# Kernel optimization log

Measured on AMD Instinct MI355X. Metric: run time of the kernel, lower is better.

Reference implementation:

```python
import jax, jax.numpy as jnp
import numpy as np
import math

B, S, D, H = 2, 2048, 1024, 16

def setup_inputs() -> dict:
    key = jax.random.key(0)
    ks = jax.random.split(key, 13)
    def lin(kw, kb, out_d, in_d):
        W = jax.random.normal(kw, (out_d, in_d), dtype=jnp.float32) * 0.02
        b = jax.random.normal(kb, (out_d,), dtype=jnp.float32) * 0.02
        return W, b
    Wq, bq = lin(ks[0], ks[1], D, D)
    Wk, bk = lin(ks[2], ks[3], D, D)
    Wv, bv = lin(ks[4], ks[5], D, D)
    Wo, bo = lin(ks[6], ks[7], D, D)
    query = jax.random.normal(ks[8], (B, S, D), dtype=jnp.float32)
    key_t = jax.random.normal(ks[9], (B, S, D), dtype=jnp.float32)
    value = jax.random.normal(ks[10], (B, S, D), dtype=jnp.float32)
    src_mask = jax.random.randint(ks[11], (B, S), 0, 2).astype(bool)  # True = masked out
    return {"query": query, "key": key_t, "value": value, "src_mask": src_mask,
            "Wq": Wq, "bq": bq, "Wk": Wk, "bk": bk, "Wv": Wv, "bv": bv,
            "Wo": Wo, "bo": bo, "nhead": H}

def reference(query, key, value, src_mask, Wq, bq, Wk, bk, Wv, bv, Wo, bo, nhead):
    b, s, d = query.shape
    hd = d // nhead
    scale = 1.0 / math.sqrt(hd)
    def split_heads(x):  # [b,s,d] -> [b,h,s,hd]
        return x.reshape(b, -1, nhead, hd).transpose(0, 2, 1, 3)
    q = split_heads(query @ Wq.T + bq)
    k = split_heads(key @ Wk.T + bk)
    v = split_heads(value @ Wv.T + bv)
    scores = jnp.einsum('bhqe,bhke->bhqk', q, k) * scale  # [b,h,s,s]
    # mask True -> -9e9, broadcast over heads and query positions (matches repeat)
    scores = jnp.where(src_mask[:, None, None, :], jnp.float32(-9e9), scores)
    probs = jax.nn.softmax(scores, axis=-1)
    # dropout is identity in eval mode
    out = jnp.einsum('bhqk,bhke->bhqe', probs, v)  # [b,h,s,hd]
    out = out.transpose(0, 2, 1, 3).reshape(b, s, d)
    out = out @ Wo.T + bo
    return out
```

## Files before the change

### kernel.cpp

```cpp
#include <hip/hip_runtime.h>
#include <hip/hip_bf16.h>
#include <cstdint>
#include <cstddef>

#define B_ 2
#define S_ 2048
#define D_ 1024
#define H_ 16
#define HD_ 64
#define M_ 4096

typedef __attribute__((ext_vector_type(8))) short short8;
typedef __attribute__((ext_vector_type(4))) short shortx4;
typedef __attribute__((ext_vector_type(4))) float floatx4;

__device__ __forceinline__ floatx4 mfma32(short8 a, short8 b, floatx4 c) {
    return __builtin_amdgcn_mfma_f32_16x16x32_bf16(a, b, c, 0, 0, 0);
}
__device__ __forceinline__ floatx4 mfma16(shortx4 a, shortx4 b, floatx4 c) {
    return __builtin_amdgcn_mfma_f32_16x16x16bf16_1k(a, b, c, 0, 0, 0);
}

__device__ __forceinline__ void gload_lds16(const __hip_bfloat16* g, __hip_bfloat16* lds_base) {
    __builtin_amdgcn_global_load_lds(
        (const __attribute__((address_space(1))) void*)g,
        (__attribute__((address_space(3))) void*)lds_base, 16, 0, 0);
}

__global__ __launch_bounds__(256) void cvt_all_kernel(
    const float* __restrict__ q, const float* __restrict__ k, const float* __restrict__ v,
    const float* __restrict__ wq, const float* __restrict__ wk,
    const float* __restrict__ wv, const float* __restrict__ wo,
    __hip_bfloat16* __restrict__ dst_in,
    __hip_bfloat16* __restrict__ dst_w)
{
    const size_t SZ_IN = (size_t)M_ * D_;
    const size_t SZ_W  = (size_t)D_ * D_;
    int i = (blockIdx.x * 256 + threadIdx.x) * 4;
    const float* src;
    __hip_bfloat16* d;
    if (blockIdx.z < 3) {
        src = blockIdx.z == 0 ? q : blockIdx.z == 1 ? k : v;
        d = dst_in + (size_t)blockIdx.z * SZ_IN + i;
        src += i;
    } else {
        int w = i >> 20;
        int off = i & (int)(SZ_W - 1);
        src = (w == 0 ? wq : w == 1 ? wk : w == 2 ? wv : wo) + off;
        d = dst_w + (size_t)w * SZ_W + off;
    }
    float4 vv = *(const float4*)src;
    union { __hip_bfloat16 h[4]; uint2 u; } cv;
    cv.h[0] = __float2bfloat16(vv.x); cv.h[1] = __float2bfloat16(vv.y);
    cv.h[2] = __float2bfloat16(vv.z); cv.h[3] = __float2bfloat16(vv.w);
    *(uint2*)d = cv.u;
}

template <int MODE>
__device__ __forceinline__ void gemm_core(
    const __hip_bfloat16* __restrict__ A,
    const __hip_bfloat16* __restrict__ W,
    const float* __restrict__ bias,
    void* __restrict__ Cout,
    __hip_bfloat16* __restrict__ smem,
    int m0, int n0, int N, float scale)
{
    __hip_bfloat16* As = smem;
    __hip_bfloat16* Bs = smem + 128 * 32;
    const int K = D_;
    const int tid  = threadIdx.x;
    const int wave = tid >> 6;
    const int lane = tid & 63;
    const int quad = lane >> 4;
    const int l15  = lane & 15;
    const int wm   = (wave & 1) * 64;
    const int wn   = (wave >> 1) * 64;
    const int srow = lane >> 2;
    const int scol = (lane & 3) * 8;

    floatx4 acc[4][4];
#pragma unroll
    for (int i = 0; i < 4; i++)
#pragma unroll
        for (int j = 0; j < 4; j++) {
            floatx4 z = {0.f, 0.f, 0.f, 0.f};
            acc[i][j] = z;
        }

    for (int k0 = 0; k0 < K; k0 += 32) {
        __syncthreads();
#pragma unroll
        for (int t = 0; t < 2; t++) {
            int r0 = wave * 32 + t * 16;
            gload_lds16(A + (size_t)(m0 + r0 + srow) * K + k0 + scol, As + r0 * 32);
            gload_lds16(W + (size_t)(n0 + r0 + srow) * K + k0 + scol, Bs + r0 * 32);
        }
        __syncthreads();

        short8 afr[4], bfr[4];
#pragma unroll
        for (int i = 0; i < 4; i++)
            afr[i] = *(const short8*)(As + (wm + i * 16 + l15) * 32 + quad * 8);
#pragma unroll
        for (int j = 0; j < 4; j++)
            bfr[j] = *(const short8*)(Bs + (wn + j * 16 + l15) * 32 + quad * 8);
#pragma unroll
        for (int i = 0; i < 4; i++)
#pragma unroll
            for (int j = 0; j < 4; j++)
                acc[i][j] = mfma32(afr[i], bfr[j], acc[i][j]);
    }

    if constexpr (MODE == 1) {
#pragma unroll
        for (int j = 0; j < 4; j++) {
            int col = n0 + wn + j * 16 + l15;
            int h = col >> 6, e = col & 63;
            float bv = bias[col];
#pragma unroll
            for (int i = 0; i < 4; i++) {
                int s0 = m0 + wm + i * 16 + quad * 4;
                int bb = s0 >> 11, sl = s0 & 2047;
                union { __hip_bfloat16 hx[4]; uint2 u; } pk;
#pragma unroll
                for (int r = 0; r < 4; r++)
                    pk.hx[r] = __float2bfloat16(acc[i][j][r] + bv);
                *(uint2*)((__hip_bfloat16*)Cout + (((size_t)bb * H_ + h) * HD_ + e) * S_ + sl) = pk.u;
            }
        }
    } else {
#pragma unroll
        for (int j = 0; j < 4; j++) {
            int col = n0 + wn + j * 16 + l15;
            float bv = bias[col];
#pragma unroll
            for (int i = 0; i < 4; i++) {
#pragma unroll
                for (int r = 0; r < 4; r++) {
                    int rowg = m0 + wm + i * 16 + quad * 4 + r;
                    ((__hip_bfloat16*)Cout)[(size_t)rowg * N + col] =
                        __float2bfloat16((acc[i][j][r] + bv) * scale);
                }
            }
        }
    }
}

__global__ __launch_bounds__(256) void qkv_gemm_kernel(
    const __hip_bfloat16* __restrict__ qb, const __hip_bfloat16* __restrict__ kb,
    const __hip_bfloat16* __restrict__ vb,
    const __hip_bfloat16* __restrict__ Wqb, const __hip_bfloat16* __restrict__ Wkb,
    const __hip_bfloat16* __restrict__ Wvb,
    const float* __restrict__ bq, const float* __restrict__ bk, const float* __restrict__ bv,
    __hip_bfloat16* __restrict__ Qp, __hip_bfloat16* __restrict__ Kp,
    __hip_bfloat16* __restrict__ Vt)
{
    __shared__ __hip_bfloat16 smem[2 * 128 * 32] __attribute__((aligned(16)));
    const int z = blockIdx.z;
    const __hip_bfloat16* A = z == 0 ? qb : z == 1 ? kb : vb;
    const __hip_bfloat16* W = z == 0 ? Wqb : z == 1 ? Wkb : Wvb;
    const float* bias = z == 0 ? bq : z == 1 ? bk : bv;
    int m0 = blockIdx.y * 128, n0 = blockIdx.x * 128;
    const float kSc = 0.18033688f;
    if (z < 2) gemm_core<0>(A, W, bias, z == 0 ? (void*)Qp : (void*)Kp, smem, m0, n0, D_,
                            z == 0 ? kSc : 1.0f);
    else       gemm_core<1>(A, W, bias, (void*)Vt, smem, m0, n0, D_, 1.0f);
}

__global__ __launch_bounds__(256) void oproj_gemm_kernel(
    const __hip_bfloat16* __restrict__ A, const __hip_bfloat16* __restrict__ W,
    const float* __restrict__ bias, float* __restrict__ out)
{
    __shared__ __hip_bfloat16 As[64 * 32]  __attribute__((aligned(16)));
    __shared__ __hip_bfloat16 Bs[128 * 32] __attribute__((aligned(16)));
    const int K = D_, N = D_;
    const int tid  = threadIdx.x;
    const int m0   = blockIdx.y * 64;
    const int n0   = blockIdx.x * 128;
    const int wave = tid >> 6;
    const int lane = tid & 63;
    const int quad = lane >> 4;
    const int l15  = lane & 15;
    const int wm   = (wave & 1) * 32;
    const int wn   = (wave >> 1) * 64;
    const int srow = lane >> 2;
    const int scol = (lane & 3) * 8;

    floatx4 acc[2][4];
#pragma unroll
    for (int i = 0; i < 2; i++)
#pragma unroll
        for (int j = 0; j < 4; j++) {
            floatx4 z = {0.f, 0.f, 0.f, 0.f};
            acc[i][j] = z;
        }

    for (int k0 = 0; k0 < K; k0 += 32) {
        __syncthreads();
        {
            int ra = wave * 16;
            gload_lds16(A + (size_t)(m0 + ra + srow) * K + k0 + scol, As + ra * 32);
#pragma unroll
            for (int t = 0; t < 2; t++) {
                int rb = wave * 32 + t * 16;
                gload_lds16(W + (size_t)(n0 + rb + srow) * K + k0 + scol, Bs + rb * 32);
            }
        }
        __syncthreads();

        short8 afr[2], bfr[4];
#pragma unroll
        for (int i = 0; i < 2; i++)
            afr[i] = *(const short8*)(As + (wm + i * 16 + l15) * 32 + quad * 8);
#pragma unroll
        for (int j = 0; j < 4; j++)
            bfr[j] = *(const short8*)(Bs + (wn + j * 16 + l15) * 32 + quad * 8);
#pragma unroll
        for (int i = 0; i < 2; i++)
#pragma unroll
            for (int j = 0; j < 4; j++)
                acc[i][j] = mfma32(afr[i], bfr[j], acc[i][j]);
    }

#pragma unroll
    for (int j = 0; j < 4; j++) {
        int col = n0 + wn + j * 16 + l15;
        float bv = bias[col];
#pragma unroll
        for (int i = 0; i < 2; i++) {
#pragma unroll
            for (int r = 0; r < 4; r++) {
                int rowg = m0 + wm + i * 16 + quad * 4 + r;
                out[(size_t)rowg * N + col] = acc[i][j][r] + bv;
            }
        }
    }
}

#define LDP 72
__global__ __launch_bounds__(512) void flash_attn_kernel(
    const __hip_bfloat16* __restrict__ Q,
    const __hip_bfloat16* __restrict__ Kp,
    const __hip_bfloat16* __restrict__ Vt,
    const int* __restrict__ mask,
    __hip_bfloat16* __restrict__ O)
{
    __shared__ __hip_bfloat16 Qs [128 * LDP] __attribute__((aligned(16)));
    __shared__ __hip_bfloat16 Ks [64 * LDP]  __attribute__((aligned(16)));
    __shared__ __hip_bfloat16 Vts[64 * LDP]  __attribute__((aligned(16)));

    const int tid  = threadIdx.x;
    const int q0   = blockIdx.x * 128;
    const int bh   = blockIdx.y;
    const int b    = bh >> 4;
    const int h    = bh & 15;
    const int wave = tid >> 6;
    const int lane = tid & 63;
    const int quad = lane >> 4;
    const int l15  = lane & 15;

    const size_t baseQ = ((size_t)b * S_ + q0) * D_ + (size_t)h * HD_;
#pragma unroll
    for (int c = tid; c < 1024; c += 512) {
        int row = c >> 3, kc = c & 7;
        *(uint4*)(Qs + row * LDP + kc * 8) = *(const uint4*)(Q + baseQ + (size_t)row * D_ + kc * 8);
    }
    __syncthreads();

    short8 qb[2];
    qb[0] = *(const short8*)(Qs + (wave * 16 + l15) * LDP + quad * 8);
    qb[1] = *(const short8*)(Qs + (wave * 16 + l15) * LDP + 32 + quad * 8);

    const shortx4 ones = {(short)0x3F80, (short)0x3F80, (short)0x3F80, (short)0x3F80};
    floatx4 l_acc = {0.f, 0.f, 0.f, 0.f};
    floatx4 o_acc[4];
#pragma unroll
    for (int ot = 0; ot < 4; ot++) {
        floatx4 z = {0.f, 0.f, 0.f, 0.f};
        o_acc[ot] = z;
    }

    const int* mrow = mask + b * S_;
    const __hip_bfloat16* VtBase = Vt + (size_t)bh * HD_ * S_;

    for (int kv0 = 0; kv0 < S_; kv0 += 64) {
        __syncthreads();
        const size_t baseK = ((size_t)b * S_ + kv0) * D_ + (size_t)h * HD_;
        {
            int row = tid >> 3, kc = tid & 7;
            *(uint4*)(Ks + row * LDP + kc * 8) =
                *(const uint4*)(Kp + baseK + (size_t)row * D_ + kc * 8);
            *(uint4*)(Vts + row * LDP + kc * 8) =
                *(const uint4*)(VtBase + (size_t)row * S_ + kv0 + kc * 8);
        }
        __syncthreads();

        int4 mq[4];
#pragma unroll
        for (int nt = 0; nt < 4; nt++)
            mq[nt] = *(const int4*)(mrow + kv0 + nt * 16 + quad * 4);

        floatx4 s_acc[4];
#pragma unroll
        for (int nt = 0; nt < 4; nt++) {
            short8 kb0 = *(const short8*)(Ks + (nt * 16 + l15) * LDP + quad * 8);
            short8 kb1 = *(const short8*)(Ks + (nt * 16 + l15) * LDP + 32 + quad * 8);
            floatx4 z = {0.f, 0.f, 0.f, 0.f};
            z = mfma32(kb0, qb[0], z);
            z = mfma32(kb1, qb[1], z);
            s_acc[nt] = z;
        }

        shortx4 pf[4];
#pragma unroll
        for (int nt = 0; nt < 4; nt++) {
            float pe0 = mq[nt].x ? 0.f : __builtin_amdgcn_exp2f(s_acc[nt][0]);
            float pe1 = mq[nt].y ? 0.f : __builtin_amdgcn_exp2f(s_acc[nt][1]);
            float pe2 = mq[nt].z ? 0.f : __builtin_amdgcn_exp2f(s_acc[nt][2]);
            float pe3 = mq[nt].w ? 0.f : __builtin_amdgcn_exp2f(s_acc[nt][3]);
            union { shortx4 s4; __hip_bfloat162 b2[2]; } pk;
            pk.b2[0] = __float22bfloat162_rn({pe0, pe1});
            pk.b2[1] = __float22bfloat162_rn({pe2, pe3});
            pf[nt] = pk.s4;
        }

#pragma unroll
        for (int nt = 0; nt < 4; nt++) {
            l_acc = mfma16(pf[nt], ones, l_acc);
#pragma unroll
            for (int ot = 0; ot < 4; ot++) {
                shortx4 vb = *(const shortx4*)(Vts + (ot * 16 + l15) * LDP + nt * 16 + quad * 4);
                o_acc[ot] = mfma16(pf[nt], vb, o_acc[ot]);
            }
        }
    }

    const size_t baseO = ((size_t)b * S_ + q0) * D_ + (size_t)h * HD_;
#pragma unroll
    for (int r = 0; r < 4; r++) {
        float inv = 1.0f / l_acc[r];
        int rowl = wave * 16 + quad * 4 + r;
#pragma unroll
        for (int ot = 0; ot < 4; ot++)
            O[baseO + (size_t)rowl * D_ + ot * 16 + l15] =
                __float2bfloat16(o_acc[ot][r] * inv);
    }
}

extern "C" void kernel_launch(void* const* d_in, const int* in_sizes, int n_in,
                              void* d_out, int out_size, void* d_ws, size_t ws_size,
                              hipStream_t stream) {
    const float* query = (const float*)d_in[0];
    const float* key   = (const float*)d_in[1];
    const float* value = (const float*)d_in[2];
    const int*   mask  = (const int*)d_in[3];
    const float* Wq    = (const float*)d_in[4];
    const float* bq    = (const float*)d_in[5];
    const float* Wk    = (const float*)d_in[6];
    const float* bk    = (const float*)d_in[7];
    const float* Wv    = (const float*)d_in[8];
    const float* bv    = (const float*)d_in[9];
    const float* Wo    = (const float*)d_in[10];
    const float* bo    = (const float*)d_in[11];
    float* out = (float*)d_out;

    const size_t SZ_IN = (size_t)M_ * D_;
    const size_t SZ_W  = (size_t)D_ * D_;
    __hip_bfloat16* qb  = (__hip_bfloat16*)d_ws;
    __hip_bfloat16* kb  = qb  + SZ_IN;
    __hip_bfloat16* vb  = kb  + SZ_IN;
    __hip_bfloat16* Wqb = vb  + SZ_IN;
    __hip_bfloat16* Wkb = Wqb + SZ_W;
    __hip_bfloat16* Wvb = Wkb + SZ_W;
    __hip_bfloat16* Wob = Wvb + SZ_W;
    __hip_bfloat16* Qp  = Wob + SZ_W;
    __hip_bfloat16* Kp  = Qp  + SZ_IN;
    __hip_bfloat16* Vt  = Kp  + SZ_IN;

    cvt_all_kernel<<<dim3(SZ_IN / 1024, 1, 4), 256, 0, stream>>>(
        query, key, value, Wq, Wk, Wv, Wo, qb, Wqb);

    qkv_gemm_kernel<<<dim3(D_ / 128, M_ / 128, 3), 256, 0, stream>>>(
        qb, kb, vb, Wqb, Wkb, Wvb, bq, bk, bv, Qp, Kp, Vt);

    flash_attn_kernel<<<dim3(S_ / 128, B_ * H_), 512, 0, stream>>>(Qp, Kp, Vt, mask, Qp);

    oproj_gemm_kernel<<<dim3(D_ / 128, M_ / 64), 256, 0, stream>>>(Qp, Wob, bo, out);
}
```

Measured before the change: 247.8 us.

## Double K-step per barrier in GEMMs and compute softmax denominators with shuffles

Both projection GEMMs now load two 32-wide K slices into LDS per loop iteration, so the loop takes 64-wide K steps and executes half as many __syncthreads barriers. LDS use per block doubles in exchange. In the attention kernel, the row-sum of probabilities is no longer computed with an extra MFMA against a vector of ones. It is accumulated in fp32 registers and reduced with cross-lane shuffles at the end, which removes one MFMA per tile but adds VALU adds.

```diff
diff --git a/kernel.cpp b/kernel.cpp
--- a/kernel.cpp
+++ b/kernel.cpp
@@ -40,9 +40,8 @@
     const float* src;
     __hip_bfloat16* d;
     if (blockIdx.z < 3) {
-        src = blockIdx.z == 0 ? q : blockIdx.z == 1 ? k : v;
+        src = (blockIdx.z == 0 ? q : blockIdx.z == 1 ? k : v) + i;
         d = dst_in + (size_t)blockIdx.z * SZ_IN + i;
-        src += i;
     } else {
         int w = i >> 20;
         int off = i & (int)(SZ_W - 1);
@@ -66,7 +65,7 @@
     int m0, int n0, int N, float scale)
 {
     __hip_bfloat16* As = smem;
-    __hip_bfloat16* Bs = smem + 128 * 32;
+    __hip_bfloat16* Bs = smem + 2 * 128 * 32;
     const int K = D_;
     const int tid  = threadIdx.x;
     const int wave = tid >> 6;
@@ -87,28 +86,36 @@
             acc[i][j] = z;
         }
 
-    for (int k0 = 0; k0 < K; k0 += 32) {
-        __syncthreads();
-#pragma unroll
-        for (int t = 0; t < 2; t++) {
-            int r0 = wave * 32 + t * 16;
-            gload_lds16(A + (size_t)(m0 + r0 + srow) * K + k0 + scol, As + r0 * 32);
-            gload_lds16(W + (size_t)(n0 + r0 + srow) * K + k0 + scol, Bs + r0 * 32);
-        }
-        __syncthreads();
-
-        short8 afr[4], bfr[4];
-#pragma unroll
-        for (int i = 0; i < 4; i++)
-            afr[i] = *(const short8*)(As + (wm + i * 16 + l15) * 32 + quad * 8);
-#pragma unroll
-        for (int j = 0; j < 4; j++)
-            bfr[j] = *(const short8*)(Bs + (wn + j * 16 + l15) * 32 + quad * 8);
-#pragma unroll
-        for (int i = 0; i < 4; i++)
+    for (int k0 = 0; k0 < K; k0 += 64) {
+        __syncthreads();
+#pragma unroll
+        for (int h2 = 0; h2 < 2; h2++) {
+#pragma unroll
+            for (int t = 0; t < 2; t++) {
+                int r0 = wave * 32 + t * 16;
+                gload_lds16(A + (size_t)(m0 + r0 + srow) * K + k0 + h2 * 32 + scol,
+                            As + h2 * 4096 + r0 * 32);
+                gload_lds16(W + (size_t)(n0 + r0 + srow) * K + k0 + h2 * 32 + scol,
+                            Bs + h2 * 4096 + r0 * 32);
+            }
+        }
+        __syncthreads();
+
+#pragma unroll
+        for (int h2 = 0; h2 < 2; h2++) {
+            short8 afr[4], bfr[4];
+#pragma unroll
+            for (int i = 0; i < 4; i++)
+                afr[i] = *(const short8*)(As + h2 * 4096 + (wm + i * 16 + l15) * 32 + quad * 8);
 #pragma unroll
             for (int j = 0; j < 4; j++)
-                acc[i][j] = mfma32(afr[i], bfr[j], acc[i][j]);
+                bfr[j] = *(const short8*)(Bs + h2 * 4096 + (wn + j * 16 + l15) * 32 + quad * 8);
+#pragma unroll
+            for (int i = 0; i < 4; i++)
+#pragma unroll
+                for (int j = 0; j < 4; j++)
+                    acc[i][j] = mfma32(afr[i], bfr[j], acc[i][j]);
+        }
     }
 
     if constexpr (MODE == 1) {
@@ -155,7 +162,7 @@
     __hip_bfloat16* __restrict__ Qp, __hip_bfloat16* __restrict__ Kp,
     __hip_bfloat16* __restrict__ Vt)
 {
-    __shared__ __hip_bfloat16 smem[2 * 128 * 32] __attribute__((aligned(16)));
+    __shared__ __hip_bfloat16 smem[2 * 2 * 128 * 32] __attribute__((aligned(16)));
     const int z = blockIdx.z;
     const __hip_bfloat16* A = z == 0 ? qb : z == 1 ? kb : vb;
     const __hip_bfloat16* W = z == 0 ? Wqb : z == 1 ? Wkb : Wvb;
@@ -171,8 +178,8 @@
     const __hip_bfloat16* __restrict__ A, const __hip_bfloat16* __restrict__ W,
     const float* __restrict__ bias, float* __restrict__ out)
 {
-    __shared__ __hip_bfloat16 As[64 * 32]  __attribute__((aligned(16)));
-    __shared__ __hip_bfloat16 Bs[128 * 32] __attribute__((aligned(16)));
+    __shared__ __hip_bfloat16 As[2 * 64 * 32]  __attribute__((aligned(16)));
+    __shared__ __hip_bfloat16 Bs[2 * 128 * 32] __attribute__((aligned(16)));
     const int K = D_, N = D_;
     const int tid  = threadIdx.x;
     const int m0   = blockIdx.y * 64;
@@ -195,31 +202,37 @@
             acc[i][j] = z;
         }
 
-    for (int k0 = 0; k0 < K; k0 += 32) {
-        __syncthreads();
-        {
+    for (int k0 = 0; k0 < K; k0 += 64) {
+        __syncthreads();
+#pragma unroll
+        for (int h2 = 0; h2 < 2; h2++) {
             int ra = wave * 16;
-            gload_lds16(A + (size_t)(m0 + ra + srow) * K + k0 + scol, As + ra * 32);
+            gload_lds16(A + (size_t)(m0 + ra + srow) * K + k0 + h2 * 32 + scol,
+                        As + h2 * 2048 + ra * 32);
 #pragma unroll
             for (int t = 0; t < 2; t++) {
                 int rb = wave * 32 + t * 16;
-                gload_lds16(W + (size_t)(n0 + rb + srow) * K + k0 + scol, Bs + rb * 32);
-            }
-        }
-        __syncthreads();
-
-        short8 afr[2], bfr[4];
-#pragma unroll
-        for (int i = 0; i < 2; i++)
-            afr[i] = *(const short8*)(As + (wm + i * 16 + l15) * 32 + quad * 8);
-#pragma unroll
-        for (int j = 0; j < 4; j++)
-            bfr[j] = *(const short8*)(Bs + (wn + j * 16 + l15) * 32 + quad * 8);
-#pragma unroll
-        for (int i = 0; i < 2; i++)
+                gload_lds16(W + (size_t)(n0 + rb + srow) * K + k0 + h2 * 32 + scol,
+                            Bs + h2 * 4096 + rb * 32);
+            }
+        }
+        __syncthreads();
+
+#pragma unroll
+        for (int h2 = 0; h2 < 2; h2++) {
+            short8 afr[2], bfr[4];
+#pragma unroll
+            for (int i = 0; i < 2; i++)
+                afr[i] = *(const short8*)(As + h2 * 2048 + (wm + i * 16 + l15) * 32 + quad * 8);
 #pragma unroll
             for (int j = 0; j < 4; j++)
-                acc[i][j] = mfma32(afr[i], bfr[j], acc[i][j]);
+                bfr[j] = *(const short8*)(Bs + h2 * 4096 + (wn + j * 16 + l15) * 32 + quad * 8);
+#pragma unroll
+            for (int i = 0; i < 2; i++)
+#pragma unroll
+                for (int j = 0; j < 4; j++)
+                    acc[i][j] = mfma32(afr[i], bfr[j], acc[i][j]);
+        }
     }
 
 #pragma unroll
@@ -271,8 +284,7 @@
     qb[0] = *(const short8*)(Qs + (wave * 16 + l15) * LDP + quad * 8);
     qb[1] = *(const short8*)(Qs + (wave * 16 + l15) * LDP + 32 + quad * 8);
 
-    const shortx4 ones = {(short)0x3F80, (short)0x3F80, (short)0x3F80, (short)0x3F80};
-    floatx4 l_acc = {0.f, 0.f, 0.f, 0.f};
+    float lsum = 0.f;
     floatx4 o_acc[4];
 #pragma unroll
     for (int ot = 0; ot < 4; ot++) {
@@ -318,6 +330,7 @@
             float pe1 = mq[nt].y ? 0.f : __builtin_amdgcn_exp2f(s_acc[nt][1]);
             float pe2 = mq[nt].z ? 0.f : __builtin_amdgcn_exp2f(s_acc[nt][2]);
             float pe3 = mq[nt].w ? 0.f : __builtin_amdgcn_exp2f(s_acc[nt][3]);
+            lsum += (pe0 + pe1) + (pe2 + pe3);
             union { shortx4 s4; __hip_bfloat162 b2[2]; } pk;
             pk.b2[0] = __float22bfloat162_rn({pe0, pe1});
             pk.b2[1] = __float22bfloat162_rn({pe2, pe3});
@@ -326,7 +339,6 @@
 
 #pragma unroll
         for (int nt = 0; nt < 4; nt++) {
-            l_acc = mfma16(pf[nt], ones, l_acc);
 #pragma unroll
             for (int ot = 0; ot < 4; ot++) {
                 shortx4 vb = *(const shortx4*)(Vts + (ot * 16 + l15) * LDP + nt * 16 + quad * 4);
@@ -335,10 +347,13 @@
         }
     }
 
+    lsum += __shfl_xor(lsum, 16);
+    lsum += __shfl_xor(lsum, 32);
+
     const size_t baseO = ((size_t)b * S_ + q0) * D_ + (size_t)h * HD_;
 #pragma unroll
     for (int r = 0; r < 4; r++) {
-        float inv = 1.0f / l_acc[r];
+        float inv = 1.0f / __shfl(lsum, quad * 4 + r);
         int rowl = wave * 16 + quad * 4 + r;
 #pragma unroll
         for (int ot = 0; ot < 4; ot++)
```

Result: no change. 247.0 us (-0.3%).

## Double KV tile to 128 and replace ones-MFMA row sum with shuffle reduction

Applied to the files above, without the earlier changes.

The flash attention loop now processes 128 keys per iteration instead of 64, which halves the number of barrier-separated load phases, and it interleaves the score, exp and PV steps per 16-key subtile. The softmax denominator is no longer computed by an extra MFMA against a ones vector. Each lane instead accumulates a scalar sum of its unrounded exponentials, and cross-lane shuffles reduce it at the end. Shared memory use grows, and the denominator now sums fp32 values while the numerator uses bf16-rounded ones.

```diff
diff --git a/kernel.cpp b/kernel.cpp
--- a/kernel.cpp
+++ b/kernel.cpp
@@ -40,9 +40,8 @@
     const float* src;
     __hip_bfloat16* d;
     if (blockIdx.z < 3) {
-        src = blockIdx.z == 0 ? q : blockIdx.z == 1 ? k : v;
+        src = (blockIdx.z == 0 ? q : blockIdx.z == 1 ? k : v) + i;
         d = dst_in + (size_t)blockIdx.z * SZ_IN + i;
-        src += i;
     } else {
         int w = i >> 20;
         int off = i & (int)(SZ_W - 1);
@@ -238,6 +237,7 @@
 }
 
 #define LDP 72
+#define LDV 136
 __global__ __launch_bounds__(512) void flash_attn_kernel(
     const __hip_bfloat16* __restrict__ Q,
     const __hip_bfloat16* __restrict__ Kp,
@@ -246,8 +246,8 @@
     __hip_bfloat16* __restrict__ O)
 {
     __shared__ __hip_bfloat16 Qs [128 * LDP] __attribute__((aligned(16)));
-    __shared__ __hip_bfloat16 Ks [64 * LDP]  __attribute__((aligned(16)));
-    __shared__ __hip_bfloat16 Vts[64 * LDP]  __attribute__((aligned(16)));
+    __shared__ __hip_bfloat16 Ks [128 * LDP] __attribute__((aligned(16)));
+    __shared__ __hip_bfloat16 Vts[64 * LDV]  __attribute__((aligned(16)));
 
     const int tid  = threadIdx.x;
     const int q0   = blockIdx.x * 128;
@@ -271,8 +271,7 @@
     qb[0] = *(const short8*)(Qs + (wave * 16 + l15) * LDP + quad * 8);
     qb[1] = *(const short8*)(Qs + (wave * 16 + l15) * LDP + 32 + quad * 8);
 
-    const shortx4 ones = {(short)0x3F80, (short)0x3F80, (short)0x3F80, (short)0x3F80};
-    floatx4 l_acc = {0.f, 0.f, 0.f, 0.f};
+    float lsum = 0.f;
     floatx4 o_acc[4];
 #pragma unroll
     for (int ot = 0; ot < 4; ot++) {
@@ -283,62 +282,54 @@
     const int* mrow = mask + b * S_;
     const __hip_bfloat16* VtBase = Vt + (size_t)bh * HD_ * S_;
 
-    for (int kv0 = 0; kv0 < S_; kv0 += 64) {
+    for (int kv0 = 0; kv0 < S_; kv0 += 128) {
         __syncthreads();
         const size_t baseK = ((size_t)b * S_ + kv0) * D_ + (size_t)h * HD_;
-        {
-            int row = tid >> 3, kc = tid & 7;
-            *(uint4*)(Ks + row * LDP + kc * 8) =
-                *(const uint4*)(Kp + baseK + (size_t)row * D_ + kc * 8);
-            *(uint4*)(Vts + row * LDP + kc * 8) =
-                *(const uint4*)(VtBase + (size_t)row * S_ + kv0 + kc * 8);
-        }
-        __syncthreads();
-
-        int4 mq[4];
-#pragma unroll
-        for (int nt = 0; nt < 4; nt++)
-            mq[nt] = *(const int4*)(mrow + kv0 + nt * 16 + quad * 4);
-
-        floatx4 s_acc[4];
-#pragma unroll
-        for (int nt = 0; nt < 4; nt++) {
+#pragma unroll
+        for (int t = 0; t < 2; t++) {
+            int c = tid + t * 512;
+            int krow = c >> 3, kcol = c & 7;
+            *(uint4*)(Ks + krow * LDP + kcol * 8) =
+                *(const uint4*)(Kp + baseK + (size_t)krow * D_ + kcol * 8);
+            int vrow = c >> 4, vcol = c & 15;
+            *(uint4*)(Vts + vrow * LDV + vcol * 8) =
+                *(const uint4*)(VtBase + (size_t)vrow * S_ + kv0 + vcol * 8);
+        }
+        __syncthreads();
+
+#pragma unroll
+        for (int nt = 0; nt < 8; nt++) {
             short8 kb0 = *(const short8*)(Ks + (nt * 16 + l15) * LDP + quad * 8);
             short8 kb1 = *(const short8*)(Ks + (nt * 16 + l15) * LDP + 32 + quad * 8);
-            floatx4 z = {0.f, 0.f, 0.f, 0.f};
-            z = mfma32(kb0, qb[0], z);
-            z = mfma32(kb1, qb[1], z);
-            s_acc[nt] = z;
-        }
-
-        shortx4 pf[4];
-#pragma unroll
-        for (int nt = 0; nt < 4; nt++) {
-            float pe0 = mq[nt].x ? 0.f : __builtin_amdgcn_exp2f(s_acc[nt][0]);
-            float pe1 = mq[nt].y ? 0.f : __builtin_amdgcn_exp2f(s_acc[nt][1]);
-            float pe2 = mq[nt].z ? 0.f : __builtin_amdgcn_exp2f(s_acc[nt][2]);
-            float pe3 = mq[nt].w ? 0.f : __builtin_amdgcn_exp2f(s_acc[nt][3]);
+            floatx4 s_acc = {0.f, 0.f, 0.f, 0.f};
+            s_acc = mfma32(kb0, qb[0], s_acc);
+            s_acc = mfma32(kb1, qb[1], s_acc);
+
+            int4 mq = *(const int4*)(mrow + kv0 + nt * 16 + quad * 4);
+            float pe0 = mq.x ? 0.f : __builtin_amdgcn_exp2f(s_acc[0]);
+            float pe1 = mq.y ? 0.f : __builtin_amdgcn_exp2f(s_acc[1]);
+            float pe2 = mq.z ? 0.f : __builtin_amdgcn_exp2f(s_acc[2]);
+            float pe3 = mq.w ? 0.f : __builtin_amdgcn_exp2f(s_acc[3]);
+            lsum += (pe0 + pe1) + (pe2 + pe3);
             union { shortx4 s4; __hip_bfloat162 b2[2]; } pk;
             pk.b2[0] = __float22bfloat162_rn({pe0, pe1});
             pk.b2[1] = __float22bfloat162_rn({pe2, pe3});
-            pf[nt] = pk.s4;
-        }
-
-#pragma unroll
-        for (int nt = 0; nt < 4; nt++) {
-            l_acc = mfma16(pf[nt], ones, l_acc);
+
 #pragma unroll
             for (int ot = 0; ot < 4; ot++) {
-                shortx4 vb = *(const shortx4*)(Vts + (ot * 16 + l15) * LDP + nt * 16 + quad * 4);
-                o_acc[ot] = mfma16(pf[nt], vb, o_acc[ot]);
-            }
-        }
-    }
+                shortx4 vb = *(const shortx4*)(Vts + (ot * 16 + l15) * LDV + nt * 16 + quad * 4);
+                o_acc[ot] = mfma16(pk.s4, vb, o_acc[ot]);
+            }
+        }
+    }
+
+    lsum += __shfl_xor(lsum, 16);
+    lsum += __shfl_xor(lsum, 32);
 
     const size_t baseO = ((size_t)b * S_ + q0) * D_ + (size_t)h * HD_;
 #pragma unroll
     for (int r = 0; r < 4; r++) {
-        float inv = 1.0f / l_acc[r];
+        float inv = 1.0f / __shfl(lsum, quad * 4 + r);
         int rowl = wave * 16 + quad * 4 + r;
 #pragma unroll
         for (int ot = 0; ot < 4; ot++)
```

Measured after the change: 247.6 us. Within noise of the previous version (-0.1%).

## Double-buffer K/V tiles with register prefetch and compute row sums on VALU

Applied to the files above, without the earlier changes.

The flash attention loop now prefetches the next K/V tile into registers while the current tile is being computed, then stores it into a second LDS buffer. This replaces the two barriers per 64-key tile with one and hides global-load latency. The mask row is staged once into LDS instead of being read from global memory every tile. The softmax denominator now comes from a per-lane VALU sum plus cross-quad shuffles instead of an extra MFMA against a vector of ones. The trade-offs are more LDS per block and more registers, and the denominator is now summed from fp32 probabilities rather than the bf16-rounded ones.

```diff
diff --git a/kernel.cpp b/kernel.cpp
--- a/kernel.cpp
+++ b/kernel.cpp
@@ -40,9 +40,8 @@
     const float* src;
     __hip_bfloat16* d;
     if (blockIdx.z < 3) {
-        src = blockIdx.z == 0 ? q : blockIdx.z == 1 ? k : v;
+        src = (blockIdx.z == 0 ? q : blockIdx.z == 1 ? k : v) + i;
         d = dst_in + (size_t)blockIdx.z * SZ_IN + i;
-        src += i;
     } else {
         int w = i >> 20;
         int off = i & (int)(SZ_W - 1);
@@ -245,9 +244,10 @@
     const int* __restrict__ mask,
     __hip_bfloat16* __restrict__ O)
 {
-    __shared__ __hip_bfloat16 Qs [128 * LDP] __attribute__((aligned(16)));
-    __shared__ __hip_bfloat16 Ks [64 * LDP]  __attribute__((aligned(16)));
-    __shared__ __hip_bfloat16 Vts[64 * LDP]  __attribute__((aligned(16)));
+    __shared__ __hip_bfloat16 Qs [128 * LDP]    __attribute__((aligned(16)));
+    __shared__ __hip_bfloat16 Ks [2 * 64 * LDP] __attribute__((aligned(16)));
+    __shared__ __hip_bfloat16 Vts[2 * 64 * LDP] __attribute__((aligned(16)));
+    __shared__ int Ms[S_];
 
     const int tid  = threadIdx.x;
     const int q0   = blockIdx.x * 128;
@@ -265,14 +265,14 @@
         int row = c >> 3, kc = c & 7;
         *(uint4*)(Qs + row * LDP + kc * 8) = *(const uint4*)(Q + baseQ + (size_t)row * D_ + kc * 8);
     }
+    ((int4*)Ms)[tid] = ((const int4*)(mask + b * S_))[tid];
     __syncthreads();
 
     short8 qb[2];
     qb[0] = *(const short8*)(Qs + (wave * 16 + l15) * LDP + quad * 8);
     qb[1] = *(const short8*)(Qs + (wave * 16 + l15) * LDP + 32 + quad * 8);
 
-    const shortx4 ones = {(short)0x3F80, (short)0x3F80, (short)0x3F80, (short)0x3F80};
-    floatx4 l_acc = {0.f, 0.f, 0.f, 0.f};
+    float lsum = 0.f;
     floatx4 o_acc[4];
 #pragma unroll
     for (int ot = 0; ot < 4; ot++) {
@@ -280,65 +280,80 @@
         o_acc[ot] = z;
     }
 
-    const int* mrow = mask + b * S_;
+    const __hip_bfloat16* KpBase = Kp + (size_t)b * S_ * D_ + (size_t)h * HD_;
     const __hip_bfloat16* VtBase = Vt + (size_t)bh * HD_ * S_;
-
-    for (int kv0 = 0; kv0 < S_; kv0 += 64) {
-        __syncthreads();
-        const size_t baseK = ((size_t)b * S_ + kv0) * D_ + (size_t)h * HD_;
-        {
-            int row = tid >> 3, kc = tid & 7;
-            *(uint4*)(Ks + row * LDP + kc * 8) =
-                *(const uint4*)(Kp + baseK + (size_t)row * D_ + kc * 8);
-            *(uint4*)(Vts + row * LDP + kc * 8) =
-                *(const uint4*)(VtBase + (size_t)row * S_ + kv0 + kc * 8);
-        }
-        __syncthreads();
-
-        int4 mq[4];
-#pragma unroll
-        for (int nt = 0; nt < 4; nt++)
-            mq[nt] = *(const int4*)(mrow + kv0 + nt * 16 + quad * 4);
-
+    const int srow  = tid >> 3;
+    const int scol8 = (tid & 7) * 8;
+
+    uint4 kpre, vpre;
+    auto load_kv = [&](int kv) {
+        kpre = *(const uint4*)(KpBase + (size_t)(kv + srow) * D_ + scol8);
+        vpre = *(const uint4*)(VtBase + (size_t)srow * S_ + kv + scol8);
+    };
+    auto store_kv = [&](int buf) {
+        *(uint4*)(Ks  + buf * (64 * LDP) + srow * LDP + scol8) = kpre;
+        *(uint4*)(Vts + buf * (64 * LDP) + srow * LDP + scol8) = vpre;
+    };
+    auto compute = [&](const __hip_bfloat16* KsB, const __hip_bfloat16* VtsB, int kv0) {
         floatx4 s_acc[4];
 #pragma unroll
         for (int nt = 0; nt < 4; nt++) {
-            short8 kb0 = *(const short8*)(Ks + (nt * 16 + l15) * LDP + quad * 8);
-            short8 kb1 = *(const short8*)(Ks + (nt * 16 + l15) * LDP + 32 + quad * 8);
+            short8 kb0 = *(const short8*)(KsB + (nt * 16 + l15) * LDP + quad * 8);
+            short8 kb1 = *(const short8*)(KsB + (nt * 16 + l15) * LDP + 32 + quad * 8);
             floatx4 z = {0.f, 0.f, 0.f, 0.f};
             z = mfma32(kb0, qb[0], z);
             z = mfma32(kb1, qb[1], z);
             s_acc[nt] = z;
         }
-
         shortx4 pf[4];
 #pragma unroll
         for (int nt = 0; nt < 4; nt++) {
-            float pe0 = mq[nt].x ? 0.f : __builtin_amdgcn_exp2f(s_acc[nt][0]);
-            float pe1 = mq[nt].y ? 0.f : __builtin_amdgcn_exp2f(s_acc[nt][1]);
-            float pe2 = mq[nt].z ? 0.f : __builtin_amdgcn_exp2f(s_acc[nt][2]);
-            float pe3 = mq[nt].w ? 0.f : __builtin_amdgcn_exp2f(s_acc[nt][3]);
+            int4 mq = *(const int4*)(Ms + kv0 + nt * 16 + quad * 4);
+            float pe0 = mq.x ? 0.f : __builtin_amdgcn_exp2f(s_acc[nt][0]);
+            float pe1 = mq.y ? 0.f : __builtin_amdgcn_exp2f(s_acc[nt][1]);
+            float pe2 = mq.z ? 0.f : __builtin_amdgcn_exp2f(s_acc[nt][2]);
+            float pe3 = mq.w ? 0.f : __builtin_amdgcn_exp2f(s_acc[nt][3]);
+            lsum += (pe0 + pe1) + (pe2 + pe3);
             union { shortx4 s4; __hip_bfloat162 b2[2]; } pk;
             pk.b2[0] = __float22bfloat162_rn({pe0, pe1});
             pk.b2[1] = __float22bfloat162_rn({pe2, pe3});
             pf[nt] = pk.s4;
         }
-
 #pragma unroll
         for (int nt = 0; nt < 4; nt++) {
-            l_acc = mfma16(pf[nt], ones, l_acc);
 #pragma unroll
             for (int ot = 0; ot < 4; ot++) {
-                shortx4 vb = *(const shortx4*)(Vts + (ot * 16 + l15) * LDP + nt * 16 + quad * 4);
+                shortx4 vb = *(const shortx4*)(VtsB + (ot * 16 + l15) * LDP + nt * 16 + quad * 4);
                 o_acc[ot] = mfma16(pf[nt], vb, o_acc[ot]);
             }
         }
-    }
+    };
+
+    load_kv(0);
+    store_kv(0);
+    __syncthreads();
+
+    for (int itp = 0; itp < 16; itp++) {
+        int kv0 = itp * 128;
+        load_kv(kv0 + 64);
+        compute(Ks, Vts, kv0);
+        store_kv(1);
+        __syncthreads();
+        if (itp < 15) load_kv(kv0 + 128);
+        compute(Ks + 64 * LDP, Vts + 64 * LDP, kv0 + 64);
+        if (itp < 15) {
+            store_kv(0);
+            __syncthreads();
+        }
+    }
+
+    lsum += __shfl_xor(lsum, 16);
+    lsum += __shfl_xor(lsum, 32);
 
     const size_t baseO = ((size_t)b * S_ + q0) * D_ + (size_t)h * HD_;
 #pragma unroll
     for (int r = 0; r < 4; r++) {
-        float inv = 1.0f / l_acc[r];
+        float inv = 1.0f / __shfl(lsum, quad * 4 + r);
         int rowl = wave * 16 + quad * 4 + r;
 #pragma unroll
         for (int ot = 0; ot < 4; ot++)
```

New measurement: 244.7 us. No clear change (-1.3%).
